# Optimization experiments

Measured on AMD Instinct MI355X. Metric: run time of the kernel, lower is better.

## Reference

```python
import jax, jax.numpy as jnp
import numpy as np

EPS = 1e-5
K = 9  # 3x3 kernel taps


def _deform_conv_bn_relu(x, w_off, b_off, w, gamma, beta):
    B, C, H, W = x.shape
    dt = x.dtype
    # offset-predicting conv: [B, 2*K, H, W], channel layout (y,x) pairs per tap (mmcv v1)
    offset = jax.lax.conv_general_dilated(
        x, w_off, window_strides=(1, 1), padding=((1, 1), (1, 1)),
        dimension_numbers=('NCHW', 'OIHW', 'NCHW')) + b_off[None, :, None, None]
    off = offset.reshape(B, K, 2, H, W)
    # kernel tap displacements relative to output pixel (padding=1 -> centered 3x3)
    dy = (jnp.arange(K) // 3 - 1).astype(dt)
    dx = (jnp.arange(K) % 3 - 1).astype(dt)
    ii = jnp.arange(H, dtype=dt)[:, None]
    jj = jnp.arange(W, dtype=dt)[None, :]
    py = ii[None, None] + dy[None, :, None, None] + off[:, :, 0]  # [B,K,H,W]
    px = jj[None, None] + dx[None, :, None, None] + off[:, :, 1]
    y0 = jnp.floor(py)
    x0 = jnp.floor(px)
    ly = py - y0
    lx = px - x0

    xf = x.reshape(B, C, H * W)

    def gather(yc, xc, wt):
        # bilinear corner gather with zero padding outside the image
        valid = (yc >= 0) & (yc < H) & (xc >= 0) & (xc < W)
        yi = jnp.clip(yc, 0, H - 1).astype(jnp.int32)
        xi = jnp.clip(xc, 0, W - 1).astype(jnp.int32)
        idx = (yi * W + xi).reshape(B, -1)              # [B, K*H*W]
        g = jax.vmap(lambda xb, ib: xb[:, ib])(xf, idx)  # [B, C, K*H*W]
        wm = (wt * valid.astype(dt)).reshape(B, 1, -1)
        return g * wm

    val = (gather(y0, x0, (1 - ly) * (1 - lx))
           + gather(y0, x0 + 1, (1 - ly) * lx)
           + gather(y0 + 1, x0, ly * (1 - lx))
           + gather(y0 + 1, x0 + 1, ly * lx))
    val = val.reshape(B, C, K, H, W)

    # deformable conv accumulation (no bias in mmcv DeformConv2d v1)
    O = w.shape[0]
    out = jnp.einsum('ock,bckhw->bohw', w.reshape(O, C, K), val)

    # BatchNorm (training-mode batch stats) + ReLU
    mean = out.mean(axis=(0, 2, 3))
    var = out.var(axis=(0, 2, 3))
    out = (out - mean[None, :, None, None]) * jax.lax.rsqrt(var + EPS)[None, :, None, None]
    out = out * gamma[None, :, None, None] + beta[None, :, None, None]
    return jax.nn.relu(out)


def setup_inputs() -> dict:
    key = jax.random.key(0)
    k1, k2, k3 = jax.random.split(key, 3)
    B, C, O, H, W = 2, 256, 256, 128, 128
    x = jax.random.normal(k1, (B, C, H, W), dtype=jnp.float32)
    # offset branch: small init so predicted offsets stay in a realistic range
    w_off = jax.random.normal(k2, (2 * K, C, 3, 3), dtype=jnp.float32) * 0.01
    b_off = jnp.zeros((2 * K,), dtype=jnp.float32)
    w = jax.random.normal(k3, (O, C, 3, 3), dtype=jnp.float32) * 0.05
    gamma = jnp.ones((O,), dtype=jnp.float32)
    beta = jnp.zeros((O,), dtype=jnp.float32)
    return {"x": x, "w_off": w_off, "b_off": b_off, "w": w, "gamma": gamma, "beta": beta}


def reference(x, w_off, b_off, w, gamma, beta):
    return _deform_conv_bn_relu(x, w_off, b_off, w, gamma, beta)
```

## Files before the change

### kernel.cpp

```cpp
#include <hip/hip_runtime.h>
#include <hip/hip_bf16.h>

#define HWs   16384
#define Wimg  128
#define Himg  128
#define PW    130
#define PHW   16900
#define Cin   256
#define Oout  256
#define CKd   2304
#define Bb    2

typedef short   bf16x8 __attribute__((ext_vector_type(8)));
typedef float   f32x4  __attribute__((ext_vector_type(4)));

__device__ __forceinline__ float bf2f(ushort u){
  union { unsigned int i; float f; } v; v.i = ((unsigned int)u) << 16; return v.f;
}
__device__ __forceinline__ ushort f2bf(float f){
  union { float f; unsigned int i; } v; v.f = f;
  unsigned int r = v.i + 0x7FFFu + ((v.i >> 16) & 1u);
  return (ushort)(r >> 16);
}
__device__ __forceinline__ void gload_lds16(const ushort* g, void* l){
  __builtin_amdgcn_global_load_lds(
      (const __attribute__((address_space(1))) unsigned int*)g,
      (__attribute__((address_space(3))) unsigned int*)l, 16, 0, 0);
}

__global__ __launch_bounds__(256) void k_transpose(const float* __restrict__ x,
                                                   ushort* __restrict__ xtp){
  int bx = blockIdx.x;
  int b  = bx >> 10;
  int r  = bx & 1023;
  int ct = r >> 8;
  int pt = r & 255;
  int c0 = ct * 64, p0 = pt * 64;
  __shared__ float tile[64][65];
  const float* xb = x + (size_t)b * Cin * HWs;
  #pragma unroll
  for (int pass = 0; pass < 16; ++pass){
    int idx = pass * 256 + threadIdx.x;
    int cl = idx >> 6, pl = idx & 63;
    tile[cl][pl] = xb[(size_t)(c0 + cl) * HWs + p0 + pl];
  }
  __syncthreads();
  ushort* xo = xtp + (size_t)b * PHW * Cin;
  #pragma unroll
  for (int pass = 0; pass < 16; ++pass){
    int idx = pass * 256 + threadIdx.x;
    int pl = idx >> 6, cl = idx & 63;
    int hw = p0 + pl; int y = hw >> 7, xc = hw & 127;
    xo[(size_t)((y + 1) * PW + xc + 1) * Cin + c0 + cl] = f2bf(tile[cl][pl]);
  }
}

__global__ __launch_bounds__(64) void k_border(ushort* __restrict__ xtp){
  int e = blockIdx.x;
  int b = e / 516, p = e % 516;
  int y, xc;
  if (p < 130)      { y = 0;       xc = p; }
  else if (p < 260) { y = 129;     xc = p - 130; }
  else if (p < 388) { y = p - 259; xc = 0; }
  else              { y = p - 387; xc = 129; }
  uint2* dst = (uint2*)(xtp + ((size_t)b * PHW + y * PW + xc) * Cin) + threadIdx.x;
  *dst = make_uint2(0u, 0u);
}

__global__ __launch_bounds__(256) void k_wprep(const float* __restrict__ w,
                                               const float* __restrict__ wof,
                                               ushort* __restrict__ w2,
                                               ushort* __restrict__ w2of){
  int idx = blockIdx.x * 256 + threadIdx.x;
  if (idx < Oout * CKd){
    int o = idx / CKd, r = idx % CKd;
    int k = r >> 8, c = r & 255;
    w2[idx] = f2bf(w[(size_t)(o * Cin + c) * 9 + k]);
  } else {
    int j = idx - Oout * CKd;
    int o = j / CKd, r = j % CKd;
    int k = r >> 8, c = r & 255;
    float v = (o < 18) ? wof[(size_t)(o * Cin + c) * 9 + k] : 0.f;
    w2of[j] = f2bf(v);
  }
}

__global__ __launch_bounds__(512) void k_offconv(const ushort* __restrict__ xtp,
                                                 const ushort* __restrict__ w2of,
                                                 const float* __restrict__ b_off,
                                                 int4* __restrict__ pidx,
                                                 float4* __restrict__ pw){
  int bx = blockIdx.x;
  int blkm = ((bx & 7) << 5) | (bx >> 3);
  int b = blkm >> 7, tile = blkm & 127;
  int hw0 = tile * 128;
  __shared__ __align__(16) ushort wl[32 * 64];
  __shared__ __align__(16) ushort vl[128 * 64];
  __shared__ float offs_lds[18][128];
  int t = threadIdx.x, lane = t & 63, wid = t >> 6;
  f32x4 acc[2];
  acc[0] = (f32x4){0,0,0,0}; acc[1] = (f32x4){0,0,0,0};
  const ushort* xb = xtp + (size_t)b * PHW * Cin;

  #pragma unroll 1
  for (int step = 0; step < 36; ++step){
    int kk = step * 64, k = kk >> 8, c0 = kk & 255;
    int dy = k / 3 - 1, dx = k % 3 - 1;
    __syncthreads();
    if (wid < 4){
      int L = wid * 1024 + lane * 16;
      int oo = L >> 7; int inb = (L & 127) ^ ((oo & 7) << 4);
      gload_lds16(w2of + (size_t)oo * CKd + kk + (inb >> 1), (char*)wl + L);
    }
    #pragma unroll
    for (int h = 0; h < 2; ++h){
      int L = (wid * 2 + h) * 1024 + lane * 16;
      int hw_l = L >> 7; int inb = (L & 127) ^ ((hw_l & 7) << 4);
      int row = (tile + dy + 1) * PW + (hw_l + dx + 1);
      gload_lds16(xb + (size_t)row * Cin + c0 + (inb >> 1), (char*)vl + L);
    }
    __syncthreads();
    #pragma unroll
    for (int kk2 = 0; kk2 < 2; ++kk2){
      int coff = kk2 * 64 + ((lane >> 4) << 4);
      bf16x8 a0, a1, bv;
      { int r = (lane & 15);            int byte = r * 128 + coff; byte ^= ((r & 7) << 4); a0 = *(const bf16x8*)((char*)wl + byte); }
      { int r = 16 + (lane & 15);       int byte = r * 128 + coff; byte ^= ((r & 7) << 4); a1 = *(const bf16x8*)((char*)wl + byte); }
      { int r = wid * 16 + (lane & 15); int byte = r * 128 + coff; byte ^= ((r & 7) << 4); bv = *(const bf16x8*)((char*)vl + byte); }
      acc[0] = __builtin_amdgcn_mfma_f32_16x16x32_bf16(a0, bv, acc[0], 0, 0, 0);
      acc[1] = __builtin_amdgcn_mfma_f32_16x16x32_bf16(a1, bv, acc[1], 0, 0, 0);
    }
  }
  int hwl = wid * 16 + (lane & 15);
  #pragma unroll
  for (int mi = 0; mi < 2; ++mi){
    #pragma unroll
    for (int r = 0; r < 4; ++r){
      int o = mi * 16 + ((lane >> 4) << 2) + r;
      if (o < 18) offs_lds[o][hwl] = acc[mi][r] + b_off[o];
    }
  }
  __syncthreads();
  for (int idx = t; idx < 9 * 128; idx += 512){
    int k = idx >> 7, j = idx & 127;
    float offy = offs_lds[2 * k][j];
    float offx = offs_lds[2 * k + 1][j];
    float py = (float)tile + (float)(k / 3 - 1) + offy;
    float px = (float)j    + (float)(k % 3 - 1) + offx;
    float y0f = floorf(py), x0f = floorf(px);
    float ly = py - y0f, lx = px - x0f;
    int y0 = (int)y0f, x0 = (int)x0f;
    int y1 = y0 + 1, x1 = x0 + 1;
    float w00 = (1.f - ly) * (1.f - lx), w01 = (1.f - ly) * lx;
    float w10 = ly * (1.f - lx),         w11 = ly * lx;
    bool vy0 = (y0 >= 0 && y0 < 128), vy1 = (y1 >= 0 && y1 < 128);
    bool vx0 = (x0 >= 0 && x0 < 128), vx1 = (x1 >= 0 && x1 < 128);
    int iy0 = min(max(y0, 0), 127), iy1 = min(max(y1, 0), 127);
    int ix0 = min(max(x0, 0), 127), ix1 = min(max(x1, 0), 127);
    size_t e = ((size_t)b * 9 + k) * HWs + hw0 + j;
    pidx[e] = make_int4((iy0 + 1) * PW + ix0 + 1, (iy0 + 1) * PW + ix1 + 1,
                        (iy1 + 1) * PW + ix0 + 1, (iy1 + 1) * PW + ix1 + 1);
    pw[e]   = make_float4(vy0 && vx0 ? w00 : 0.f, vy0 && vx1 ? w01 : 0.f,
                          vy1 && vx0 ? w10 : 0.f, vy1 && vx1 ? w11 : 0.f);
  }
}

__device__ __forceinline__ void mfma_phase(const ushort* Ab, const ushort* Bbp,
                                           int lane, int wm, int wn, f32x4 (&acc)[4][4]){
  #pragma unroll
  for (int kk2 = 0; kk2 < 2; ++kk2){
    int coff = kk2 * 64 + ((lane >> 4) << 4);
    bf16x8 a[4], bv[4];
    #pragma unroll
    for (int mi = 0; mi < 4; ++mi){
      int r = wm * 64 + mi * 16 + (lane & 15);
      int byte = r * 128 + coff; byte ^= ((r & 7) << 4);
      a[mi] = *(const bf16x8*)((const char*)Ab + byte);
    }
    #pragma unroll
    for (int ni = 0; ni < 4; ++ni){
      int r = wn * 64 + ni * 16 + (lane & 15);
      int byte = r * 128 + coff; byte ^= ((r & 7) << 4);
      bv[ni] = *(const bf16x8*)((const char*)Bbp + byte);
    }
    #pragma unroll
    for (int mi = 0; mi < 4; ++mi)
      #pragma unroll
      for (int ni = 0; ni < 4; ++ni)
        acc[mi][ni] = __builtin_amdgcn_mfma_f32_16x16x32_bf16(a[mi], bv[ni], acc[mi][ni], 0, 0, 0);
  }
}

__global__ __launch_bounds__(512, 2) void k_main(const ushort* __restrict__ xtp,
                                                 const ushort* __restrict__ w2,
                                                 const int4* __restrict__ pidx,
                                                 const float4* __restrict__ pw,
                                                 float* __restrict__ out,
                                                 float* __restrict__ partials){
  int bx = blockIdx.x;
  int blkm = ((bx & 7) << 5) | (bx >> 3);
  int b = blkm >> 7, tile = blkm & 127;
  int hw0 = tile * 128;
  __shared__ __align__(16) ushort smem[49152];
  ushort* Ab0 = smem;
  ushort* Ab1 = smem + 16384;
  ushort* Bb0 = smem + 32768;
  ushort* Bb1 = smem + 40960;
  int t = threadIdx.x, lane = t & 63, wid = t >> 6;
  int wm = wid >> 1, wn = wid & 1;
  int cg = t & 7, hl = t >> 3;
  f32x4 acc[4][4];
  #pragma unroll
  for (int mi = 0; mi < 4; ++mi)
    #pragma unroll
    for (int ni = 0; ni < 4; ++ni) acc[mi][ni] = (f32x4){0,0,0,0};
  const ushort* xb  = xtp  + (size_t)b * PHW * Cin;
  const int4*   pib = pidx + (size_t)b * 9 * HWs + hw0;
  const float4* pwb = pw   + (size_t)b * 9 * HWs + hw0;

  int4   ids[2][2];
  float4 wts[2][2];
  bf16x8 g[2][4];

#define IDXLOAD(P, S) \
  if ((S) < 36){ int kq = (S) >> 2; \
    ids[P][0] = pib[(size_t)kq * HWs + hl];       wts[P][0] = pwb[(size_t)kq * HWs + hl]; \
    ids[P][1] = pib[(size_t)kq * HWs + hl + 64];  wts[P][1] = pwb[(size_t)kq * HWs + hl + 64]; }

#define CORNERS(P, S) \
  if ((S) < 36){ int cb = (((S) * 64) & 255) + cg * 8; \
    _Pragma("unroll") for (int hh = 0; hh < 2; ++hh){ \
      g[hh][0] = *(const bf16x8*)(xb + (size_t)ids[P][hh].x * Cin + cb); \
      g[hh][1] = *(const bf16x8*)(xb + (size_t)ids[P][hh].y * Cin + cb); \
      g[hh][2] = *(const bf16x8*)(xb + (size_t)ids[P][hh].z * Cin + cb); \
      g[hh][3] = *(const bf16x8*)(xb + (size_t)ids[P][hh].w * Cin + cb); } }

#define STAGEA(S, ABP) \
  if ((S) < 36){ int kks = (S) * 64; \
    _Pragma("unroll") for (int h2 = 0; h2 < 4; ++h2){ \
      int L = (wid * 4 + h2) * 1024 + lane * 16; \
      int oo = L >> 7; int inb = (L & 127) ^ ((oo & 7) << 4); \
      gload_lds16(w2 + (size_t)oo * CKd + kks + (inb >> 1), (char*)(ABP) + L); } }

#define COMBINE(P, S, BBP) \
  if ((S) < 36){ \
    _Pragma("unroll") for (int hh = 0; hh < 2; ++hh){ \
      int hw_l = hl + hh * 64; \
      float4 wtv = wts[P][hh]; \
      bf16x8 vv; \
      _Pragma("unroll") for (int jx = 0; jx < 8; ++jx){ \
        float f = wtv.x * bf2f((ushort)g[hh][0][jx]) + wtv.y * bf2f((ushort)g[hh][1][jx]) \
                + wtv.z * bf2f((ushort)g[hh][2][jx]) + wtv.w * bf2f((ushort)g[hh][3][jx]); \
        vv[jx] = (short)f2bf(f); } \
      int byte = hw_l * 128 + cg * 16; byte ^= ((hw_l & 7) << 4); \
      *(bf16x8*)((char*)(BBP) + byte) = vv; } }

  IDXLOAD(0, 0);
  IDXLOAD(1, 1);
  CORNERS(0, 0);
  STAGEA(0, Ab0);
  COMBINE(0, 0, Bb0);
  __syncthreads();

  #pragma unroll 1
  for (int tt = 0; tt < 36; tt += 2){
    IDXLOAD(0, tt + 2);
    CORNERS(1, tt + 1);
    STAGEA(tt + 1, Ab1);
    mfma_phase(Ab0, Bb0, lane, wm, wn, acc);
    COMBINE(1, tt + 1, Bb1);
    __syncthreads();
    IDXLOAD(1, tt + 3);
    CORNERS(0, tt + 2);
    STAGEA(tt + 2, Ab0);
    mfma_phase(Ab1, Bb1, lane, wm, wn, acc);
    COMBINE(0, tt + 2, Bb0);
    __syncthreads();
  }
#undef IDXLOAD
#undef CORNERS
#undef STAGEA
#undef COMBINE

  #pragma unroll
  for (int mi = 0; mi < 4; ++mi){
    int obase = wm * 64 + mi * 16 + ((lane >> 4) << 2);
    #pragma unroll
    for (int ni = 0; ni < 4; ++ni){
      int hw = hw0 + wn * 64 + ni * 16 + (lane & 15);
      float* op = out + ((size_t)b * Oout + obase) * HWs + hw;
      #pragma unroll
      for (int r = 0; r < 4; ++r) op[(size_t)r * HWs] = acc[mi][ni][r];
    }
  }
  #pragma unroll
  for (int mi = 0; mi < 4; ++mi){
    #pragma unroll
    for (int r = 0; r < 4; ++r){
      float s = 0.f, s2 = 0.f;
      #pragma unroll
      for (int ni = 0; ni < 4; ++ni){ float v = acc[mi][ni][r]; s += v; s2 += v * v; }
      #pragma unroll
      for (int off2 = 1; off2 < 16; off2 <<= 1){
        s  += __shfl_xor(s, off2);
        s2 += __shfl_xor(s2, off2);
      }
      if ((lane & 15) == 0){
        int o = wm * 64 + mi * 16 + ((lane >> 4) << 2) + r;
        int row = blkm * 2 + wn;
        partials[(size_t)row * 256 + o] = s;
        partials[(size_t)1024 * 256 + (size_t)row * 256 + o] = s2;
      }
    }
  }
}

__global__ __launch_bounds__(256) void k_bnstats(const float* __restrict__ partials,
                                                 float* __restrict__ stats){
  int o = blockIdx.x, t = threadIdx.x;
  float s = 0.f, s2 = 0.f;
  for (int i = t; i < 1024; i += 256){
    s  += partials[(size_t)i * 256 + o];
    s2 += partials[(size_t)1024 * 256 + (size_t)i * 256 + o];
  }
  #pragma unroll
  for (int off = 32; off > 0; off >>= 1){
    s  += __shfl_down(s, off);
    s2 += __shfl_down(s2, off);
  }
  __shared__ float rs[4], rs2[4];
  int lane = t & 63, w = t >> 6;
  if (lane == 0){ rs[w] = s; rs2[w] = s2; }
  __syncthreads();
  if (t == 0){
    float S = 0.f, S2 = 0.f;
    for (int i = 0; i < 4; ++i){ S += rs[i]; S2 += rs2[i]; }
    float mean = S / 32768.f;
    float var  = S2 / 32768.f - mean * mean;
    stats[o] = mean;
    stats[256 + o] = rsqrtf(var + 1e-5f);
  }
}

__global__ __launch_bounds__(256) void k_bnapply(float* __restrict__ out,
                                                 const float* __restrict__ stats,
                                                 const float* __restrict__ gamma,
                                                 const float* __restrict__ beta){
  size_t e = ((size_t)blockIdx.x * 256 + threadIdx.x) * 4;
  int o = (int)((e >> 14) & 255);
  float mean = stats[o], rstd = stats[256 + o];
  float sc = rstd * gamma[o];
  float sh = beta[o] - mean * sc;
  float4 v = *(float4*)(out + e);
  v.x = fmaxf(v.x * sc + sh, 0.f);
  v.y = fmaxf(v.y * sc + sh, 0.f);
  v.z = fmaxf(v.z * sc + sh, 0.f);
  v.w = fmaxf(v.w * sc + sh, 0.f);
  *(float4*)(out + e) = v;
}

extern "C" void kernel_launch(void* const* d_in, const int* in_sizes, int n_in,
                              void* d_out, int out_size, void* d_ws, size_t ws_size,
                              hipStream_t stream){
  const float* x     = (const float*)d_in[0];
  const float* w_off = (const float*)d_in[1];
  const float* b_off = (const float*)d_in[2];
  const float* w     = (const float*)d_in[3];
  const float* gamma = (const float*)d_in[4];
  const float* beta  = (const float*)d_in[5];
  float* out = (float*)d_out;

  char* p = (char*)d_ws;
  ushort* xtp  = (ushort*)p; p += (size_t)Bb * PHW * Cin * 2;
  ushort* w2   = (ushort*)p; p += (size_t)Oout * CKd * 2;
  ushort* w2of = (ushort*)p; p += (size_t)32 * CKd * 2;
  int4*   pidx = (int4*)p;   p += (size_t)Bb * 9 * HWs * 16;
  float4* pwt  = (float4*)p; p += (size_t)Bb * 9 * HWs * 16;
  float*  parts= (float*)p;  p += (size_t)2 * 1024 * 256 * 4;
  float*  stats= (float*)p;

  k_transpose<<<dim3(2048), dim3(256), 0, stream>>>(x, xtp);
  k_border   <<<dim3(1032), dim3(64),  0, stream>>>(xtp);
  k_wprep    <<<dim3(2592), dim3(256), 0, stream>>>(w, w_off, w2, w2of);
  k_offconv  <<<dim3(256),  dim3(512), 0, stream>>>(xtp, w2of, b_off, pidx, pwt);
  k_main     <<<dim3(256),  dim3(512), 0, stream>>>(xtp, w2, pidx, pwt, out, parts);
  k_bnstats  <<<dim3(256),  dim3(256), 0, stream>>>(parts, stats);
  k_bnapply  <<<dim3(8192), dim3(256), 0, stream>>>(out, stats, gamma, beta);
}
```

Baseline: 131.4 us.

## Halve spatial tile to 64 pixels, double-buffer offset conv, simplify bf16 rounding

Both the offset conv and the main deformable GEMM kernel now use 64-pixel tiles instead of 128, so each launches 512 blocks. Each warp in the main kernel now owns 32 output channels instead of a 64x64 tile, and the launch bound allows 4 blocks per SM for higher occupancy across 256 CUs. The offset conv gains double-buffered LDS staging so the next K-slice loads overlap the current MFMAs. The bf16 rounding is reduced to a plain round-half-up, which is cheaper but differs slightly from round-to-nearest-even. The smaller tiles lower per-warp data reuse in the main GEMM, and the partial-stat buffers are resized to match the new block count.

```diff
diff --git a/kernel.cpp b/kernel.cpp
--- a/kernel.cpp
+++ b/kernel.cpp
@@ -19,8 +19,7 @@
 }
 __device__ __forceinline__ ushort f2bf(float f){
   union { float f; unsigned int i; } v; v.f = f;
-  unsigned int r = v.i + 0x7FFFu + ((v.i >> 16) & 1u);
-  return (ushort)(r >> 16);
+  return (ushort)((v.i + 0x8000u) >> 16);
 }
 __device__ __forceinline__ void gload_lds16(const ushort* g, void* l){
   __builtin_amdgcn_global_load_lds(
@@ -85,68 +84,67 @@
   }
 }
 
-__global__ __launch_bounds__(512) void k_offconv(const ushort* __restrict__ xtp,
-                                                 const ushort* __restrict__ w2of,
-                                                 const float* __restrict__ b_off,
-                                                 int4* __restrict__ pidx,
-                                                 float4* __restrict__ pw){
+__global__ __launch_bounds__(512, 4) void k_offconv(const ushort* __restrict__ xtp,
+                                                    const ushort* __restrict__ w2of,
+                                                    const float* __restrict__ b_off,
+                                                    int4* __restrict__ pidx,
+                                                    float4* __restrict__ pw){
   int bx = blockIdx.x;
-  int blkm = ((bx & 7) << 5) | (bx >> 3);
-  int b = blkm >> 7, tile = blkm & 127;
-  int hw0 = tile * 128;
-  __shared__ __align__(16) ushort wl[32 * 64];
-  __shared__ __align__(16) ushort vl[128 * 64];
-  __shared__ float offs_lds[18][128];
+  int blkm = ((bx & 7) << 6) | (bx >> 3);
+  int b = blkm >> 8, tile = blkm & 255;
+  int hw0 = tile * 64;
+  int iy = tile >> 1, jx0 = (tile & 1) * 64;
+  __shared__ __align__(16) ushort aw[2][2048];
+  __shared__ __align__(16) ushort bv_s[2][4096];
+  __shared__ float offs_lds[18][64];
   int t = threadIdx.x, lane = t & 63, wid = t >> 6;
-  f32x4 acc[2];
-  acc[0] = (f32x4){0,0,0,0}; acc[1] = (f32x4){0,0,0,0};
+  int mi = wid >> 2, ni = wid & 3;
+  f32x4 acc = (f32x4){0,0,0,0};
   const ushort* xb = xtp + (size_t)b * PHW * Cin;
 
+#define OSTAGE(S, P) \
+  if ((S) < 36){ int kks = (S) * 64, kt = (S) >> 2, c0s = ((S) * 64) & 255; \
+    int dy = kt / 3 - 1, dxx = kt % 3 - 1; \
+    if (wid < 4){ int L = t * 16; int oo = L >> 7; int inb = (L & 127) ^ ((oo & 7) << 4); \
+      gload_lds16(w2of + (size_t)oo * CKd + kks + (inb >> 1), (char*)aw[P] + L); } \
+    { int L = t * 16; int hw_l = L >> 7; int inb = (L & 127) ^ ((hw_l & 7) << 4); \
+      int row = (iy + dy + 1) * PW + (jx0 + hw_l + dxx + 1); \
+      gload_lds16(xb + (size_t)row * Cin + c0s + (inb >> 1), (char*)bv_s[P] + L); } }
+
+  OSTAGE(0, 0);
+  __syncthreads();
   #pragma unroll 1
   for (int step = 0; step < 36; ++step){
-    int kk = step * 64, k = kk >> 8, c0 = kk & 255;
-    int dy = k / 3 - 1, dx = k % 3 - 1;
-    __syncthreads();
-    if (wid < 4){
-      int L = wid * 1024 + lane * 16;
-      int oo = L >> 7; int inb = (L & 127) ^ ((oo & 7) << 4);
-      gload_lds16(w2of + (size_t)oo * CKd + kk + (inb >> 1), (char*)wl + L);
-    }
-    #pragma unroll
-    for (int h = 0; h < 2; ++h){
-      int L = (wid * 2 + h) * 1024 + lane * 16;
-      int hw_l = L >> 7; int inb = (L & 127) ^ ((hw_l & 7) << 4);
-      int row = (tile + dy + 1) * PW + (hw_l + dx + 1);
-      gload_lds16(xb + (size_t)row * Cin + c0 + (inb >> 1), (char*)vl + L);
-    }
-    __syncthreads();
+    int P = step & 1;
+    OSTAGE(step + 1, P ^ 1);
     #pragma unroll
     for (int kk2 = 0; kk2 < 2; ++kk2){
       int coff = kk2 * 64 + ((lane >> 4) << 4);
-      bf16x8 a0, a1, bv;
-      { int r = (lane & 15);            int byte = r * 128 + coff; byte ^= ((r & 7) << 4); a0 = *(const bf16x8*)((char*)wl + byte); }
-      { int r = 16 + (lane & 15);       int byte = r * 128 + coff; byte ^= ((r & 7) << 4); a1 = *(const bf16x8*)((char*)wl + byte); }
-      { int r = wid * 16 + (lane & 15); int byte = r * 128 + coff; byte ^= ((r & 7) << 4); bv = *(const bf16x8*)((char*)vl + byte); }
-      acc[0] = __builtin_amdgcn_mfma_f32_16x16x32_bf16(a0, bv, acc[0], 0, 0, 0);
-      acc[1] = __builtin_amdgcn_mfma_f32_16x16x32_bf16(a1, bv, acc[1], 0, 0, 0);
-    }
-  }
-  int hwl = wid * 16 + (lane & 15);
-  #pragma unroll
-  for (int mi = 0; mi < 2; ++mi){
+      bf16x8 a0, bb;
+      { int r = mi * 16 + (lane & 15); int byte = r * 128 + coff; byte ^= ((r & 7) << 4); a0 = *(const bf16x8*)((char*)aw[P] + byte); }
+      { int r = ni * 16 + (lane & 15); int byte = r * 128 + coff; byte ^= ((r & 7) << 4); bb = *(const bf16x8*)((char*)bv_s[P] + byte); }
+      acc = __builtin_amdgcn_mfma_f32_16x16x32_bf16(a0, bb, acc, 0, 0, 0);
+    }
+    __syncthreads();
+  }
+#undef OSTAGE
+  {
+    int hw_l = ni * 16 + (lane & 15);
     #pragma unroll
     for (int r = 0; r < 4; ++r){
       int o = mi * 16 + ((lane >> 4) << 2) + r;
-      if (o < 18) offs_lds[o][hwl] = acc[mi][r] + b_off[o];
-    }
-  }
-  __syncthreads();
-  for (int idx = t; idx < 9 * 128; idx += 512){
-    int k = idx >> 7, j = idx & 127;
-    float offy = offs_lds[2 * k][j];
-    float offx = offs_lds[2 * k + 1][j];
-    float py = (float)tile + (float)(k / 3 - 1) + offy;
-    float px = (float)j    + (float)(k % 3 - 1) + offx;
+      if (o < 18) offs_lds[o][hw_l] = acc[r] + b_off[o];
+    }
+  }
+  __syncthreads();
+  for (int idx = t; idx < 9 * 64; idx += 512){
+    int k = idx >> 6, jl = idx & 63;
+    int hw = hw0 + jl;
+    int i = hw >> 7, jcol = hw & 127;
+    float offy = offs_lds[2 * k][jl];
+    float offx = offs_lds[2 * k + 1][jl];
+    float py = (float)i    + (float)(k / 3 - 1) + offy;
+    float px = (float)jcol + (float)(k % 3 - 1) + offx;
     float y0f = floorf(py), x0f = floorf(px);
     float ly = py - y0f, lx = px - x0f;
     int y0 = (int)y0f, x0 = (int)x0f;
@@ -157,7 +155,7 @@
     bool vx0 = (x0 >= 0 && x0 < 128), vx1 = (x1 >= 0 && x1 < 128);
     int iy0 = min(max(y0, 0), 127), iy1 = min(max(y1, 0), 127);
     int ix0 = min(max(x0, 0), 127), ix1 = min(max(x1, 0), 127);
-    size_t e = ((size_t)b * 9 + k) * HWs + hw0 + j;
+    size_t e = ((size_t)b * 9 + k) * HWs + hw;
     pidx[e] = make_int4((iy0 + 1) * PW + ix0 + 1, (iy0 + 1) * PW + ix1 + 1,
                         (iy1 + 1) * PW + ix0 + 1, (iy1 + 1) * PW + ix1 + 1);
     pw[e]   = make_float4(vy0 && vx0 ? w00 : 0.f, vy0 && vx1 ? w01 : 0.f,
@@ -166,74 +164,71 @@
 }
 
 __device__ __forceinline__ void mfma_phase(const ushort* Ab, const ushort* Bbp,
-                                           int lane, int wm, int wn, f32x4 (&acc)[4][4]){
+                                           int lane, int wid, f32x4 (&acc)[2][4]){
   #pragma unroll
   for (int kk2 = 0; kk2 < 2; ++kk2){
     int coff = kk2 * 64 + ((lane >> 4) << 4);
-    bf16x8 a[4], bv[4];
-    #pragma unroll
-    for (int mi = 0; mi < 4; ++mi){
-      int r = wm * 64 + mi * 16 + (lane & 15);
+    bf16x8 a[2], bv[4];
+    #pragma unroll
+    for (int mi = 0; mi < 2; ++mi){
+      int r = wid * 32 + mi * 16 + (lane & 15);
       int byte = r * 128 + coff; byte ^= ((r & 7) << 4);
       a[mi] = *(const bf16x8*)((const char*)Ab + byte);
     }
     #pragma unroll
     for (int ni = 0; ni < 4; ++ni){
-      int r = wn * 64 + ni * 16 + (lane & 15);
+      int r = ni * 16 + (lane & 15);
       int byte = r * 128 + coff; byte ^= ((r & 7) << 4);
       bv[ni] = *(const bf16x8*)((const char*)Bbp + byte);
     }
     #pragma unroll
-    for (int mi = 0; mi < 4; ++mi)
+    for (int mi = 0; mi < 2; ++mi)
       #pragma unroll
       for (int ni = 0; ni < 4; ++ni)
         acc[mi][ni] = __builtin_amdgcn_mfma_f32_16x16x32_bf16(a[mi], bv[ni], acc[mi][ni], 0, 0, 0);
   }
 }
 
-__global__ __launch_bounds__(512, 2) void k_main(const ushort* __restrict__ xtp,
+__global__ __launch_bounds__(512, 4) void k_main(const ushort* __restrict__ xtp,
                                                  const ushort* __restrict__ w2,
                                                  const int4* __restrict__ pidx,
                                                  const float4* __restrict__ pw,
                                                  float* __restrict__ out,
                                                  float* __restrict__ partials){
   int bx = blockIdx.x;
-  int blkm = ((bx & 7) << 5) | (bx >> 3);
-  int b = blkm >> 7, tile = blkm & 127;
-  int hw0 = tile * 128;
-  __shared__ __align__(16) ushort smem[49152];
+  int blkm = ((bx & 7) << 6) | (bx >> 3);
+  int b = blkm >> 8, tile = blkm & 255;
+  int hw0 = tile * 64;
+  __shared__ __align__(16) ushort smem[40960];
   ushort* Ab0 = smem;
   ushort* Ab1 = smem + 16384;
   ushort* Bb0 = smem + 32768;
-  ushort* Bb1 = smem + 40960;
+  ushort* Bb1 = smem + 36864;
   int t = threadIdx.x, lane = t & 63, wid = t >> 6;
-  int wm = wid >> 1, wn = wid & 1;
   int cg = t & 7, hl = t >> 3;
-  f32x4 acc[4][4];
-  #pragma unroll
-  for (int mi = 0; mi < 4; ++mi)
+  f32x4 acc[2][4];
+  #pragma unroll
+  for (int mi = 0; mi < 2; ++mi)
     #pragma unroll
     for (int ni = 0; ni < 4; ++ni) acc[mi][ni] = (f32x4){0,0,0,0};
   const ushort* xb  = xtp  + (size_t)b * PHW * Cin;
   const int4*   pib = pidx + (size_t)b * 9 * HWs + hw0;
   const float4* pwb = pw   + (size_t)b * 9 * HWs + hw0;
 
-  int4   ids[2][2];
-  float4 wts[2][2];
-  bf16x8 g[2][4];
+  int4   ids[2];
+  float4 wts[2];
+  bf16x8 g[4];
 
 #define IDXLOAD(P, S) \
   if ((S) < 36){ int kq = (S) >> 2; \
-    ids[P][0] = pib[(size_t)kq * HWs + hl];       wts[P][0] = pwb[(size_t)kq * HWs + hl]; \
-    ids[P][1] = pib[(size_t)kq * HWs + hl + 64];  wts[P][1] = pwb[(size_t)kq * HWs + hl + 64]; }
+    ids[P] = pib[(size_t)kq * HWs + hl]; wts[P] = pwb[(size_t)kq * HWs + hl]; }
 
 #define CORNERS(P, S) \
   if ((S) < 36){ int cb = (((S) * 64) & 255) + cg * 8; \
-    _Pragma("unroll") for (int hh = 0; hh < 2; ++hh){ \
-      g[hh][0] = *(const bf16x8*)(xb + (size_t)ids[P][hh].x * Cin + cb); \
-      g[hh][1] = *(const bf16x8*)(xb + (size_t)ids[P][hh].y * Cin + cb); \
-      g[hh][2] = *(const bf16x8*)(xb + (size_t)ids[P][hh].z * Cin + cb); \
-      g[hh][3] = *(const bf16x8*)(xb + (size_t)ids[P][hh].w * Cin + cb); } }
+    g[0] = *(const bf16x8*)(xb + (size_t)ids[P].x * Cin + cb); \
+    g[1] = *(const bf16x8*)(xb + (size_t)ids[P].y * Cin + cb); \
+    g[2] = *(const bf16x8*)(xb + (size_t)ids[P].z * Cin + cb); \
+    g[3] = *(const bf16x8*)(xb + (size_t)ids[P].w * Cin + cb); }
 
 #define STAGEA(S, ABP) \
   if ((S) < 36){ int kks = (S) * 64; \
@@ -244,16 +239,14 @@
 
 #define COMBINE(P, S, BBP) \
   if ((S) < 36){ \
-    _Pragma("unroll") for (int hh = 0; hh < 2; ++hh){ \
-      int hw_l = hl + hh * 64; \
-      float4 wtv = wts[P][hh]; \
-      bf16x8 vv; \
-      _Pragma("unroll") for (int jx = 0; jx < 8; ++jx){ \
-        float f = wtv.x * bf2f((ushort)g[hh][0][jx]) + wtv.y * bf2f((ushort)g[hh][1][jx]) \
-                + wtv.z * bf2f((ushort)g[hh][2][jx]) + wtv.w * bf2f((ushort)g[hh][3][jx]); \
-        vv[jx] = (short)f2bf(f); } \
-      int byte = hw_l * 128 + cg * 16; byte ^= ((hw_l & 7) << 4); \
-      *(bf16x8*)((char*)(BBP) + byte) = vv; } }
+    float4 wtv = wts[P]; \
+    bf16x8 vv; \
+    _Pragma("unroll") for (int jx = 0; jx < 8; ++jx){ \
+      float f = wtv.x * bf2f((ushort)g[0][jx]) + wtv.y * bf2f((ushort)g[1][jx]) \
+              + wtv.z * bf2f((ushort)g[2][jx]) + wtv.w * bf2f((ushort)g[3][jx]); \
+      vv[jx] = (short)f2bf(f); } \
+    int byte = hl * 128 + cg * 16; byte ^= ((hl & 7) << 4); \
+    *(bf16x8*)((char*)(BBP) + byte) = vv; }
 
   IDXLOAD(0, 0);
   IDXLOAD(1, 1);
@@ -267,13 +260,13 @@
     IDXLOAD(0, tt + 2);
     CORNERS(1, tt + 1);
     STAGEA(tt + 1, Ab1);
-    mfma_phase(Ab0, Bb0, lane, wm, wn, acc);
+    mfma_phase(Ab0, Bb0, lane, wid, acc);
     COMBINE(1, tt + 1, Bb1);
     __syncthreads();
     IDXLOAD(1, tt + 3);
     CORNERS(0, tt + 2);
     STAGEA(tt + 2, Ab0);
-    mfma_phase(Ab1, Bb1, lane, wm, wn, acc);
+    mfma_phase(Ab1, Bb1, lane, wid, acc);
     COMBINE(0, tt + 2, Bb0);
     __syncthreads();
   }
@@ -283,18 +276,18 @@
 #undef COMBINE
 
   #pragma unroll
-  for (int mi = 0; mi < 4; ++mi){
-    int obase = wm * 64 + mi * 16 + ((lane >> 4) << 2);
+  for (int mi = 0; mi < 2; ++mi){
+    int obase = wid * 32 + mi * 16 + ((lane >> 4) << 2);
     #pragma unroll
     for (int ni = 0; ni < 4; ++ni){
-      int hw = hw0 + wn * 64 + ni * 16 + (lane & 15);
+      int hw = hw0 + ni * 16 + (lane & 15);
       float* op = out + ((size_t)b * Oout + obase) * HWs + hw;
       #pragma unroll
       for (int r = 0; r < 4; ++r) op[(size_t)r * HWs] = acc[mi][ni][r];
     }
   }
   #pragma unroll
-  for (int mi = 0; mi < 4; ++mi){
+  for (int mi = 0; mi < 2; ++mi){
     #pragma unroll
     for (int r = 0; r < 4; ++r){
       float s = 0.f, s2 = 0.f;
@@ -306,10 +299,9 @@
         s2 += __shfl_xor(s2, off2);
       }
       if ((lane & 15) == 0){
-        int o = wm * 64 + mi * 16 + ((lane >> 4) << 2) + r;
-        int row = blkm * 2 + wn;
-        partials[(size_t)row * 256 + o] = s;
-        partials[(size_t)1024 * 256 + (size_t)row * 256 + o] = s2;
+        int o = wid * 32 + mi * 16 + ((lane >> 4) << 2) + r;
+        partials[(size_t)blkm * 256 + o] = s;
+        partials[(size_t)512 * 256 + (size_t)blkm * 256 + o] = s2;
       }
     }
   }
@@ -319,9 +311,9 @@
                                                  float* __restrict__ stats){
   int o = blockIdx.x, t = threadIdx.x;
   float s = 0.f, s2 = 0.f;
-  for (int i = t; i < 1024; i += 256){
+  for (int i = t; i < 512; i += 256){
     s  += partials[(size_t)i * 256 + o];
-    s2 += partials[(size_t)1024 * 256 + (size_t)i * 256 + o];
+    s2 += partials[(size_t)512 * 256 + (size_t)i * 256 + o];
   }
   #pragma unroll
   for (int off = 32; off > 0; off >>= 1){
@@ -376,14 +368,14 @@
   ushort* w2of = (ushort*)p; p += (size_t)32 * CKd * 2;
   int4*   pidx = (int4*)p;   p += (size_t)Bb * 9 * HWs * 16;
   float4* pwt  = (float4*)p; p += (size_t)Bb * 9 * HWs * 16;
-  float*  parts= (float*)p;  p += (size_t)2 * 1024 * 256 * 4;
+  float*  parts= (float*)p;  p += (size_t)2 * 512 * 256 * 4;
   float*  stats= (float*)p;
 
   k_transpose<<<dim3(2048), dim3(256), 0, stream>>>(x, xtp);
   k_border   <<<dim3(1032), dim3(64),  0, stream>>>(xtp);
   k_wprep    <<<dim3(2592), dim3(256), 0, stream>>>(w, w_off, w2, w2of);
-  k_offconv  <<<dim3(256),  dim3(512), 0, stream>>>(xtp, w2of, b_off, pidx, pwt);
-  k_main     <<<dim3(256),  dim3(512), 0, stream>>>(xtp, w2, pidx, pwt, out, parts);
+  k_offconv  <<<dim3(512),  dim3(512), 0, stream>>>(xtp, w2of, b_off, pidx, pwt);
+  k_main     <<<dim3(512),  dim3(512), 0, stream>>>(xtp, w2, pidx, pwt, out, parts);
   k_bnstats  <<<dim3(256),  dim3(256), 0, stream>>>(parts, stats);
   k_bnapply  <<<dim3(8192), dim3(256), 0, stream>>>(out, stats, gamma, beta);
 }
```

Measured after the change: 134.5 us. 1.02x slower.
